# Performance work log

Measured on AMD Instinct MI355X. Metric: run time of the kernel, lower is better.

Reference implementation:

```python
import jax, jax.numpy as jnp
import numpy as np

THETA_GAMMA = 3.0
TRUNCATE = 4.0


def _gaussian_kernel(theta_gamma=THETA_GAMMA, truncate=TRUNCATE):
    r = int(theta_gamma * truncate + 0.5)
    x, y = np.mgrid[-r:r + 1, -r:r + 1]
    k = np.exp(-(x ** 2 + y ** 2) / (2 * theta_gamma ** 2)).astype(np.float32)
    k[r, r] = 0.0  # center zeroed, as in the original module
    return r, k


def setup_inputs() -> dict:
    key = jax.random.key(0)
    src = jax.random.normal(key, (4, 512, 512, 21), dtype=jnp.float32)
    r, k = _gaussian_kernel()
    return {"src": src, "k": jnp.asarray(k), "r": r}


def reference(src, k, r):
    # src: [bs, h, w, c]; k: [2r+1, 2r+1]
    bs, h, w, c = src.shape
    x = jnp.transpose(src, (0, 3, 1, 2))                       # [bs, c, h, w]
    x = jnp.pad(x, ((0, 0), (0, 0), (r, r), (r, r)))           # [bs, c, h+2r, w+2r]
    ext_k = jnp.pad(k, ((0, h - 1), (0, w - 1)))               # [h+2r, w+2r]
    ph, pw = h + 2 * r, w + 2 * r
    x_fft = jnp.fft.rfft2(x)                                   # [bs, c, ph, pw//2+1]
    k_fft = jnp.fft.rfft2(ext_k)                               # [ph, pw//2+1]
    dst = jnp.fft.irfft2(x_fft * k_fft[None, None], s=(ph, pw))
    dst = dst[..., 2 * r:, 2 * r:]                             # [bs, c, h, w]
    return jnp.transpose(dst, (0, 2, 3, 1)).astype(src.dtype)  # [bs, h, w, c]
```

## Files before the change

kernel.cpp:

```cpp
#include <hip/hip_runtime.h>


#define BATCH 4
#define HH 512
#define WW 512
#define CC 21
#define WC (WW * CC)
#define IMG ((size_t)HH * WC)
#define RAD 12

__device__ static constexpr float GW[25] = {
    3.3546263e-04f, 1.2038700e-03f, 3.8659300e-03f, 1.1108997e-02f, 2.8565500e-02f,
    6.5728500e-02f, 1.3533528e-01f, 2.4935221e-01f, 4.1111229e-01f, 6.0653066e-01f,
    8.0073740e-01f, 9.4595947e-01f, 1.0000000e+00f, 9.4595947e-01f, 8.0073740e-01f,
    6.0653066e-01f, 4.1111229e-01f, 2.4935221e-01f, 1.3533528e-01f, 6.5728500e-02f,
    2.8565500e-02f, 1.1108997e-02f, 3.8659300e-03f, 1.2038700e-03f, 3.3546263e-04f
};

constexpr int BH  = 4;
constexpr int NT  = 896;
constexpr int SD  = 273;
constexpr int SDR = CC * SD;
constexpr int NSV = BH + 2 * RAD;

__global__ __launch_bounds__(NT, 1)
void fused_kernel(const float* __restrict__ src, float* __restrict__ out)
{
    __shared__ unsigned int v_d[BH * SDR];
    __shared__ float out_row[WC];

    const int tid = threadIdx.x;

    const int bid  = blockIdx.x;
    const int lin  = (bid & 7) * 64 + (bid >> 3);
    const int b    = lin >> 7;
    const int i0   = (lin & 127) * BH;
    const float* sb = src + (size_t)b * IMG;

#pragma unroll
    for (int rep = 0; rep < 2; ++rep) {
        const int item = tid + rep * NT;
        if (item < BH * 21 * 17) {
            const int rowp = item / 357;
            const int m    = item % 357;
            const int c    = m / 17, mm = m % 17;
            const int jd   = (mm < 8) ? mm : (256 + mm);
            v_d[rowp * SDR + c * SD + jd] = 0u;
        }
    }

    _Float16* vh = (_Float16*)v_d;
#pragma unroll 1
    for (int cch = 0; cch < 3; ++cch) {
        const int ff = 4 * tid + 3584 * cch;
        const float* scol = sb + ff;

        float a0[BH], a1[BH], a2[BH], a3[BH];
#pragma unroll
        for (int l = 0; l < BH; ++l) { a0[l]=0.f; a1[l]=0.f; a2[l]=0.f; a3[l]=0.f; }

#pragma unroll
        for (int st = 0; st < NSV; ++st) {
            const int r = i0 - RAD + st;
            float4 x = make_float4(0.f, 0.f, 0.f, 0.f);
            if ((unsigned)r < (unsigned)HH)
                x = *(const float4*)(scol + (size_t)r * WC);
#pragma unroll
            for (int l = 0; l < BH; ++l) {
                const int t = st - l;
                if (t >= 0 && t <= 2 * RAD) {
                    const float w = GW[t];
                    a0[l] = fmaf(w, x.x, a0[l]);
                    a1[l] = fmaf(w, x.y, a1[l]);
                    a2[l] = fmaf(w, x.z, a2[l]);
                    a3[l] = fmaf(w, x.w, a3[l]);
                }
            }
        }

#pragma unroll
        for (int e = 0; e < 4; ++e) {
            const int fe = ff + e;
            const int ch = fe % CC, j = fe / CC;
            const int ofs = ch * (2 * SD) + 16 + j;
#pragma unroll
            for (int l = 0; l < BH; ++l) {
                const float av = (e == 0) ? a0[l] : (e == 1) ? a1[l]
                               : (e == 2) ? a2[l] : a3[l];
                vh[l * (2 * SDR) + ofs] = (_Float16)av;
            }
        }
    }
    __syncthreads();

#pragma unroll 1
    for (int rr = 0; rr < BH; ++rr) {
        if (tid < 672) {
            const int c  = tid % CC;
            const int j0 = (tid / CC) * 16;
            const unsigned int* vb = v_d + rr * SDR + c * SD + (j0 + 4) / 2;
            float w[40];
#pragma unroll
            for (int m = 0; m < 20; ++m) {
                union { unsigned int u; _Float16 h[2]; } cv;
                cv.u = vb[m];
                w[2 * m]     = (float)cv.h[0];
                w[2 * m + 1] = (float)cv.h[1];
            }
#pragma unroll
            for (int k = 0; k < 16; ++k) {
                float a = 0.f;
#pragma unroll
                for (int t = 0; t < 25; ++t)
                    a = fmaf(GW[t], w[k + t], a);
                out_row[(j0 + k) * CC + c] = a;
            }
        }
        __syncthreads();

        const size_t rowbase = ((size_t)b * HH + i0 + rr) * WC;
        const float4* srcv = (const float4*)(src + rowbase);
        float4*       outv = (float4*)(out + rowbase);
        const float4* olv  = (const float4*)out_row;
#pragma unroll
        for (int k2 = 0; k2 < 3; ++k2) {
            const int g = tid + k2 * NT;
            const float4 o = olv[g];
            const float4 s = srcv[g];
            outv[g] = make_float4(o.x - s.x, o.y - s.y, o.z - s.z, o.w - s.w);
        }
        __syncthreads();
    }
}

extern "C" void kernel_launch(void* const* d_in, const int* in_sizes, int n_in,
                              void* d_out, int out_size, void* d_ws, size_t ws_size,
                              hipStream_t stream)
{
    const float* src = (const float*)d_in[0];
    float*       out = (float*)d_out;
    (void)d_ws; (void)ws_size;

    dim3 g(HH / BH * BATCH);
    fused_kernel<<<g, NT, 0, stream>>>(src, out);
}
```

Before: 220.7 us.

## Stream row-tiled separable Gaussian with register ring buffer for vertical pass

Replaces the per-4-row block (vertical pass first, fp16 staging, then horizontal pass) with a streaming kernel. Each workgroup owns a 64-row by 672-float column slice and walks down the rows. Each input row is double-buffered in LDS and filtered horizontally, and the vertical 25-tap sum is accumulated in a rotating 25-entry register ring. This cuts the vertical halo re-reads (from 28 rows per 4 outputs to 88 per 64) and drops the fp16 intermediate. The cost is a barrier per row, a small horizontal halo, and heavy register use from the 50-entry accumulators.

```diff
diff --git a/kernel.cpp b/kernel.cpp
--- a/kernel.cpp
+++ b/kernel.cpp
@@ -17,119 +17,128 @@
     2.8565500e-02f, 1.1108997e-02f, 3.8659300e-03f, 1.2038700e-03f, 3.3546263e-04f
 };
 
-constexpr int BH  = 4;
-constexpr int NT  = 896;
-constexpr int SD  = 273;
-constexpr int SDR = CC * SD;
-constexpr int NSV = BH + 2 * RAD;
+constexpr int NT    = 336;
+constexpr int SH    = 64;
+constexpr int NSTEP = SH + 2 * RAD;
+constexpr int CT    = 672;
+constexpr int SLICE = CT + 2 * RAD * CC;
+constexpr int NWT   = WC / CT;
+constexpr int NST   = HH / SH;
+constexpr int NWG   = NWT * NST * BATCH;
 
-__global__ __launch_bounds__(NT, 1)
-void fused_kernel(const float* __restrict__ src, float* __restrict__ out)
+#define STEP(O) do {                                                          \
+    const int st = base + (O);                                                \
+    if (st < NSTEP) {                                                         \
+        const int grh = row0 + st - RAD;            \
+        {            \
+            const int grs = grh + 1;                                          \
+            if ((unsigned)grs < HH) {                                         \
+                const float* srow = sbase + (size_t)grs * WC;                 \
+                _Pragma("unroll")                                             \
+                for (int m = 0; m < 2; ++m) {                                 \
+                    const int i2 = tid + m * NT;                              \
+                    if (i2 < SLICE / 2) {                                     \
+                        const int gf = wt672 - RAD * CC + 2 * i2;             \
+                        float2 vv = make_float2(0.f, 0.f);                    \
+                        if ((unsigned)gf < WC)                                \
+                            vv = *(const float2*)(srow + gf);                 \
+                        *(float2*)&sb[(st + 1) & 1][2 * i2] = vv;             \
+                    }                                                         \
+                }                                                             \
+            }                                                                 \
+        }                                                                     \
+        if ((unsigned)grh < HH) {         \
+            const float* sbc = &sb[st & 1][ib];                               \
+            float h0 = 0.f, h1 = 0.f;                                         \
+            float xp = sbc[0];                                                \
+            _Pragma("unroll")                                                 \
+            for (int k = 0; k < 25; ++k) {                                    \
+                const float xn = sbc[(k + 1) * CC];                           \
+                h0 = fmaf(GW[k], xp, h0);                                     \
+                h1 = fmaf(GW[k], xn, h1);                                     \
+                xp = xn;                                                      \
+            }                                                                 \
+            hb[st & 1][ib]      = h0;                                         \
+            hb[st & 1][ib + CC] = h1;                                         \
+        }                                                                     \
+        __syncthreads();                                                      \
+        if ((unsigned)grh < HH) {            \
+            const float2 hv = *(const float2*)&hb[st & 1][2 * tid];           \
+            _Pragma("unroll")                                                 \
+            for (int q = 0; q < 25; ++q) {                                    \
+                const float w = GW[(((O) - q) + 25) % 25];                    \
+                if (q == (O)) {                \
+                    r0[q] = GW[0] * hv.x;                                     \
+                    r1[q] = GW[0] * hv.y;                                     \
+                } else {                                                      \
+                    r0[q] = fmaf(w, hv.x, r0[q]);                             \
+                    r1[q] = fmaf(w, hv.y, r1[q]);                             \
+                }                                                             \
+            }                                                                 \
+        }                                                                     \
+        if (st >= 24) {                   \
+            constexpr int qd = ((O) + 1) % 25;                                \
+            const int gro = row0 + st - 24;                                   \
+            const size_t ob = ((size_t)b * HH + gro) * WC + wt672 + 2 * tid;  \
+            const float2 sv = *(const float2*)(src + ob);                     \
+            float2 ov;                                                        \
+            ov.x = r0[qd] - sv.x;                                             \
+            ov.y = r1[qd] - sv.y;                                             \
+            *(float2*)(out + ob) = ov;                                        \
+        }                                                                     \
+    }                                                                         \
+} while (0)
+
+__global__ __launch_bounds__(NT, 3)
+void gauss_stream_kernel(const float* __restrict__ src, float* __restrict__ out)
 {
-    __shared__ unsigned int v_d[BH * SDR];
-    __shared__ float out_row[WC];
+    __shared__ float sb[2][SLICE];
+    __shared__ float hb[2][CT];
 
     const int tid = threadIdx.x;
 
-    const int bid  = blockIdx.x;
-    const int lin  = (bid & 7) * 64 + (bid >> 3);
-    const int b    = lin >> 7;
-    const int i0   = (lin & 127) * BH;
-    const float* sb = src + (size_t)b * IMG;
+    const int bid = blockIdx.x;
+    const int g   = (bid & 7) * (NWG / 8) + (bid >> 3);
+    const int b   = g >> 7;
+    const int rem = g & 127;
+    const int row0  = (rem >> 4) * SH;
+    const int wt672 = (rem & 15) * CT;
+    const float* sbase = src + (size_t)b * IMG;
 
+    const int c  = tid % CC;
+    const int wg = tid / CC;
+    const int ib = wg * 42 + c;
+
+    float r0[25], r1[25];
 #pragma unroll
-    for (int rep = 0; rep < 2; ++rep) {
-        const int item = tid + rep * NT;
-        if (item < BH * 21 * 17) {
-            const int rowp = item / 357;
-            const int m    = item % 357;
-            const int c    = m / 17, mm = m % 17;
-            const int jd   = (mm < 8) ? mm : (256 + mm);
-            v_d[rowp * SDR + c * SD + jd] = 0u;
-        }
-    }
+    for (int q = 0; q < 25; ++q) { r0[q] = 0.f; r1[q] = 0.f; }
 
-    _Float16* vh = (_Float16*)v_d;
-#pragma unroll 1
-    for (int cch = 0; cch < 3; ++cch) {
-        const int ff = 4 * tid + 3584 * cch;
-        const float* scol = sb + ff;
-
-        float a0[BH], a1[BH], a2[BH], a3[BH];
+    {
+        const int grow = row0 - RAD;
+        if ((unsigned)grow < HH) {
+            const float* srow = sbase + (size_t)grow * WC;
 #pragma unroll
-        for (int l = 0; l < BH; ++l) { a0[l]=0.f; a1[l]=0.f; a2[l]=0.f; a3[l]=0.f; }
-
-#pragma unroll
-        for (int st = 0; st < NSV; ++st) {
-            const int r = i0 - RAD + st;
-            float4 x = make_float4(0.f, 0.f, 0.f, 0.f);
-            if ((unsigned)r < (unsigned)HH)
-                x = *(const float4*)(scol + (size_t)r * WC);
-#pragma unroll
-            for (int l = 0; l < BH; ++l) {
-                const int t = st - l;
-                if (t >= 0 && t <= 2 * RAD) {
-                    const float w = GW[t];
-                    a0[l] = fmaf(w, x.x, a0[l]);
-                    a1[l] = fmaf(w, x.y, a1[l]);
-                    a2[l] = fmaf(w, x.z, a2[l]);
-                    a3[l] = fmaf(w, x.w, a3[l]);
+            for (int m = 0; m < 2; ++m) {
+                const int i2 = tid + m * NT;
+                if (i2 < SLICE / 2) {
+                    const int gf = wt672 - RAD * CC + 2 * i2;
+                    float2 vv = make_float2(0.f, 0.f);
+                    if ((unsigned)gf < WC)
+                        vv = *(const float2*)(srow + gf);
+                    *(float2*)&sb[0][2 * i2] = vv;
                 }
-            }
-        }
-
-#pragma unroll
-        for (int e = 0; e < 4; ++e) {
-            const int fe = ff + e;
-            const int ch = fe % CC, j = fe / CC;
-            const int ofs = ch * (2 * SD) + 16 + j;
-#pragma unroll
-            for (int l = 0; l < BH; ++l) {
-                const float av = (e == 0) ? a0[l] : (e == 1) ? a1[l]
-                               : (e == 2) ? a2[l] : a3[l];
-                vh[l * (2 * SDR) + ofs] = (_Float16)av;
             }
         }
     }
     __syncthreads();
 
 #pragma unroll 1
-    for (int rr = 0; rr < BH; ++rr) {
-        if (tid < 672) {
-            const int c  = tid % CC;
-            const int j0 = (tid / CC) * 16;
-            const unsigned int* vb = v_d + rr * SDR + c * SD + (j0 + 4) / 2;
-            float w[40];
-#pragma unroll
-            for (int m = 0; m < 20; ++m) {
-                union { unsigned int u; _Float16 h[2]; } cv;
-                cv.u = vb[m];
-                w[2 * m]     = (float)cv.h[0];
-                w[2 * m + 1] = (float)cv.h[1];
-            }
-#pragma unroll
-            for (int k = 0; k < 16; ++k) {
-                float a = 0.f;
-#pragma unroll
-                for (int t = 0; t < 25; ++t)
-                    a = fmaf(GW[t], w[k + t], a);
-                out_row[(j0 + k) * CC + c] = a;
-            }
-        }
-        __syncthreads();
-
-        const size_t rowbase = ((size_t)b * HH + i0 + rr) * WC;
-        const float4* srcv = (const float4*)(src + rowbase);
-        float4*       outv = (float4*)(out + rowbase);
-        const float4* olv  = (const float4*)out_row;
-#pragma unroll
-        for (int k2 = 0; k2 < 3; ++k2) {
-            const int g = tid + k2 * NT;
-            const float4 o = olv[g];
-            const float4 s = srcv[g];
-            outv[g] = make_float4(o.x - s.x, o.y - s.y, o.z - s.z, o.w - s.w);
-        }
-        __syncthreads();
+    for (int base = 0; base < NSTEP; base += 25) {
+        STEP(0);  STEP(1);  STEP(2);  STEP(3);  STEP(4);
+        STEP(5);  STEP(6);  STEP(7);  STEP(8);  STEP(9);
+        STEP(10); STEP(11); STEP(12); STEP(13); STEP(14);
+        STEP(15); STEP(16); STEP(17); STEP(18); STEP(19);
+        STEP(20); STEP(21); STEP(22); STEP(23); STEP(24);
     }
 }
 
@@ -141,6 +150,5 @@
     float*       out = (float*)d_out;
     (void)d_ws; (void)ws_size;
 
-    dim3 g(HH / BH * BATCH);
-    fused_kernel<<<g, NT, 0, stream>>>(src, out);
+    gauss_stream_kernel<<<dim3(NWG), NT, 0, stream>>>(src, out);
 }
```

Result: slower. 396.0 us (+79.4%).
